# Performance work log

Hardware: AMD Instinct MI355X
Metric: run time of the kernel (lower is better)

The kernel has to match this reference:

```python
import jax, jax.numpy as jnp
import numpy as np

B, Cin, H, W = 8, 256, 32, 32
KS, NH, K = 32, 8, 5          # key_size == value_size, num_heads, kernel_size
STRIDE, PAD = 1, 2
Cout = KS * 3 * NH            # 768
EPS = 1e-5


def setup_inputs() -> dict:
    key = jax.random.key(0)
    k0, k1, k2 = jax.random.split(key, 3)
    return {
        "x": jax.random.normal(k0, (B, Cin, H, W), jnp.float32),
        "conv_w": jax.random.normal(k1, (Cout, Cin), jnp.float32) / np.sqrt(Cin).astype(np.float32),
        "conv_b": jax.random.normal(k2, (Cout,), jnp.float32) * 0.02,
        "gn_w": jnp.ones((Cout,), jnp.float32),
        "gn_b": jnp.zeros((Cout,), jnp.float32),
    }


def reference(x, conv_w, conv_b, gn_w, gn_b):
    Bb = x.shape[0]
    OH = (H + 2 * PAD - K) // STRIDE + 1
    OW = (W + 2 * PAD - K) // STRIDE + 1

    # 1x1 conv: (B, Cout, H, W)
    attn = jnp.einsum('bchw,oc->bohw', x, conv_w) + conv_b[None, :, None, None]

    # unfold / Tile2d -> (B, KH, KW, Cout, OH, OW)
    ap = jnp.pad(attn, ((0, 0), (0, 0), (PAD, PAD), (PAD, PAD)))
    rows = []
    for kh in range(K):
        cols = [ap[:, :, kh:kh + OH * STRIDE:STRIDE, kw:kw + OW * STRIDE:STRIDE]
                for kw in range(K)]
        rows.append(jnp.stack(cols, axis=1))          # (B, KW, C, OH, OW)
    tiles = jnp.stack(rows, axis=1)                   # (B, KH, KW, C, OH, OW)

    # GroupNorm over (group_channels, OH, OW) per (b, kh, kw) sample.
    # groups = 3*NH, group size = KS (each head's key/query/value chunk).
    G = 3 * NH
    t = tiles.reshape(Bb, K, K, G, KS, OH, OW)
    mean = t.mean(axis=(4, 5, 6), keepdims=True)
    var = t.var(axis=(4, 5, 6), keepdims=True)        # biased, like torch GroupNorm
    t = (t - mean) * jax.lax.rsqrt(var + EPS)
    t = t.reshape(Bb, K, K, Cout, OH, OW)
    t = t * gn_w[None, None, None, :, None, None] + gn_b[None, None, None, :, None, None]

    # (B, OH, OW, NH, 3*KS, KH*KW)
    t = t.transpose(0, 4, 5, 3, 1, 2).reshape(Bb, OH, OW, NH, 3 * KS, K * K)
    keyt = t[..., :KS, :]            # (B, OH, OW, NH, KS, KK)
    qt = t[..., KS:2 * KS, :]
    vt = t[..., 2 * KS:, :]          # (B, OH, OW, NH, VS, KK)

    q = qt.mean(axis=-1)             # mean query over the window: (B, OH, OW, NH, KS)
    sal = jnp.einsum('bijnk,bijnkp->bijnp', q, keyt) / np.float32(np.sqrt(KS))
    mask = jax.nn.softmax(sal, axis=-1)               # (B, OH, OW, NH, KK)
    out = jnp.einsum('bijnvp,bijnp->bijnv', vt, mask)  # (B, OH, OW, NH, VS)

    out = out.transpose(0, 3, 4, 1, 2).reshape(Bb, NH * KS, OH, OW)
    return out
```

## Files before the change

kernel.cpp:

```cpp
#include <hip/hip_runtime.h>
#include <hip/hip_bf16.h>

#define B_    8
#define CIN   256
#define COUT  768
#define G_    24
#define PW    40
#define PLANE 1440
#define EPS_  1e-5f

typedef float f32x4 __attribute__((ext_vector_type(4)));
typedef short s16x8 __attribute__((ext_vector_type(8)));
typedef unsigned short ushort_t;
typedef unsigned short u16x4 __attribute__((ext_vector_type(4)));
typedef unsigned long long ull_t;

#define LDS_FENCE() do { asm volatile("" ::: "memory"); \
                         __builtin_amdgcn_s_waitcnt(0xC07F); \
                         asm volatile("" ::: "memory"); } while (0)

static __device__ __forceinline__ ushort_t f2bf(float f) {
    union { float f; unsigned u; } a; a.f = f;
    const unsigned u = a.u;
    const unsigned r = u + 0x7FFFu + ((u >> 16) & 1u);
    return (ushort_t)(r >> 16);
}
static __device__ __forceinline__ float bf2f(ushort_t h) {
    union { unsigned u; float f; } a; a.u = ((unsigned)h) << 16; return a.f;
}
static __device__ __forceinline__ void st4(float* dst, u16x4 v) {
    *(f32x4*)dst = f32x4{ bf2f(v[0]), bf2f(v[1]), bf2f(v[2]), bf2f(v[3]) };
}
static __device__ __forceinline__ unsigned pk2(float lo, float hi) {
    return (unsigned)f2bf(lo) | ((unsigned)f2bf(hi) << 16);
}

__launch_bounds__(256)
__global__ void conv_gemm(const float* __restrict__ wsrc, const float* __restrict__ x,
                          const float* __restrict__ bias, ushort_t* __restrict__ attn,
                          float* __restrict__ rowAgg) {
    const int t = threadIdx.x;
    const int wv = t >> 6, lane = t & 63;
    const int q = lane >> 4, l15 = lane & 15;
    const int m0 = blockIdx.y * 64;
    const int mw = wv * 16;
    const int n_t = blockIdx.x * 64;
    const int b = n_t >> 10, nl0 = n_t & 1023;
    const int y0 = nl0 >> 5;

    __shared__ ushort_t Bs[64][264];
    ushort_t (*Ct)[2][44] = (ushort_t (*)[2][44])(&Bs[0][0]);
    float (*red)[11]      = (float (*)[11])((char*)(&Bs[0][0]) + 64 * 2 * 44 * 2);

    {
        const int half = t >> 7;
        const int kp = t & 127;
        const int k2 = kp * 2;
        const float* xr0 = x + (size_t)b * (CIN * 1024) + (size_t)k2 * 1024 + nl0 + half * 32;
        const float* xr1 = xr0 + 1024;
        #pragma unroll
        for (int c = 0; c < 8; ++c) {
            const float4 u0 = *(const float4*)(xr0 + c * 4);
            const float4 u1 = *(const float4*)(xr1 + c * 4);
            const int nn = half * 32 + c * 4;
            *(unsigned*)&Bs[nn + 0][k2] = pk2(u0.x, u1.x);
            *(unsigned*)&Bs[nn + 1][k2] = pk2(u0.y, u1.y);
            *(unsigned*)&Bs[nn + 2][k2] = pk2(u0.z, u1.z);
            *(unsigned*)&Bs[nn + 3][k2] = pk2(u0.w, u1.w);
        }
    }
    __syncthreads();

    const float* aPf = wsrc + (size_t)(m0 + mw + l15) * 256 + q * 8;

    f32x4 acc[4] = {{0,0,0,0},{0,0,0,0},{0,0,0,0},{0,0,0,0}};
    #pragma unroll
    for (int k0 = 0; k0 < 256; k0 += 32) {
        const float4 af0 = *(const float4*)(aPf + k0);
        const float4 af1 = *(const float4*)(aPf + k0 + 4);
        s16x8 a;
        a[0] = (short)f2bf(af0.x); a[1] = (short)f2bf(af0.y);
        a[2] = (short)f2bf(af0.z); a[3] = (short)f2bf(af0.w);
        a[4] = (short)f2bf(af1.x); a[5] = (short)f2bf(af1.y);
        a[6] = (short)f2bf(af1.z); a[7] = (short)f2bf(af1.w);
        const int kk = k0 + q * 8;
        const s16x8 b0 = *(const s16x8*)&Bs[l15 +  0][kk];
        const s16x8 b1 = *(const s16x8*)&Bs[l15 + 16][kk];
        const s16x8 b2 = *(const s16x8*)&Bs[l15 + 32][kk];
        const s16x8 b3 = *(const s16x8*)&Bs[l15 + 48][kk];
        acc[0] = __builtin_amdgcn_mfma_f32_16x16x32_bf16(a, b0, acc[0], 0, 0, 0);
        acc[1] = __builtin_amdgcn_mfma_f32_16x16x32_bf16(a, b1, acc[1], 0, 0, 0);
        acc[2] = __builtin_amdgcn_mfma_f32_16x16x32_bf16(a, b2, acc[2], 0, 0, 0);
        acc[3] = __builtin_amdgcn_mfma_f32_16x16x32_bf16(a, b3, acc[3], 0, 0, 0);
    }
    __syncthreads();

    float bb[4];
    #pragma unroll
    for (int r = 0; r < 4; ++r) bb[r] = bias[m0 + mw + q * 4 + r];
    #pragma unroll
    for (int j = 0; j < 4; ++j) {
        const int yy = j >> 1, xx = (j & 1) * 16 + l15;
        #pragma unroll
        for (int r = 0; r < 4; ++r)
            Ct[mw + q * 4 + r][yy][2 + xx] = f2bf(acc[j][r] + bb[r]);
    }
    #pragma unroll
    for (int it = 0; it < 2; ++it) {
        const int id = it * 256 + t;
        const int m = id >> 3, yy = (id >> 2) & 1, pos = id & 3;
        const int us = (pos == 0) ? 0 : (32 + 2 * pos);
        *(unsigned*)&Ct[m][yy][us] = 0u;
    }
    __syncthreads();

    ushort_t* pb = attn + ((size_t)(b * COUT + m0)) * PLANE;
    #pragma unroll
    for (int it = 0; it < 5; ++it) {
        const int id = it * 256 + t;
        const int m = id / 20, rem = id % 20, yy = rem / 10, s = rem % 10;
        const ull_t v = *(const ull_t*)&Ct[m][yy][s * 4];
        *(ull_t*)(pb + (size_t)m * PLANE + (y0 + yy + 2) * PW + s * 4) = v;
    }
    if (y0 == 0 || y0 == 30) {
        const int rowA = (y0 == 0) ? 0 : 34;
        #pragma unroll
        for (int it = 0; it < 5; ++it) {
            const int id = it * 256 + t;
            const int m = id / 20, rem = id % 20, yy = rem / 10, s = rem % 10;
            *(ull_t*)(pb + (size_t)m * PLANE + (rowA + yy) * PW + s * 4) = 0ull;
        }
    }

    if (t < 128) {
        const int gi = t >> 6, yy = (t >> 5) & 1, c = t & 31;
        const int m = gi * 32 + c;
        float lin = 0.f, sq = 0.f, e0 = 0.f, e1 = 0.f, e30 = 0.f, e31 = 0.f;
        #pragma unroll
        for (int u = 0; u < 9; ++u) {
            const ull_t vv = *(const ull_t*)&Ct[m][yy][u * 4];
            const unsigned lo = (unsigned)vv, hi = (unsigned)(vv >> 32);
            union { unsigned u; float f; } f0, f1, f2, f3;
            f0.u = lo << 16; f1.u = lo & 0xffff0000u;
            f2.u = hi << 16; f3.u = hi & 0xffff0000u;
            lin += (f0.f + f1.f) + (f2.f + f3.f);
            sq  += (f0.f * f0.f + f1.f * f1.f) + (f2.f * f2.f + f3.f * f3.f);
            if (u == 0) { e0 = f2.f; e1 = f3.f; }
            if (u == 8) { e30 = f0.f; e31 = f1.f; }
        }
        red[t][0] = lin; red[t][1] = sq;
        red[t][2] = e0;  red[t][3] = e0 * e0;
        red[t][4] = e1;  red[t][5] = e1 * e1;
        red[t][6] = e30; red[t][7] = e30 * e30;
        red[t][8] = e31; red[t][9] = e31 * e31;
    }
    __syncthreads();
    if (t < 40) {
        const int s = t % 10, gy = t / 10;
        const int gi = gy >> 1, yy = gy & 1;
        float sum = 0.f;
        #pragma unroll
        for (int c = 0; c < 32; ++c) sum += red[gi * 64 + yy * 32 + c][s];
        const int g = blockIdx.y * 2 + gi;
        rowAgg[(((size_t)b * G_ + g) * 32 + (y0 + yy)) * 10 + s] = sum;
    }
}

__launch_bounds__(128)
__global__ void local_attn(const ushort_t* __restrict__ attn,
                           const float* __restrict__ rowAgg,
                           const float* __restrict__ gn_w, const float* __restrict__ gn_b,
                           float* __restrict__ out) {
    const int wid = blockIdx.x;
    const int b = wid >> 7;
    const int n = (wid >> 4) & 7;
    const int i0 = (wid & 15) * 2;
    const int t = threadIdx.x;
    const int h = t >> 6;
    const int lane = t & 63;
    const int r = lane >> 5;
    const int j = lane & 31;

    __shared__ float KB[2][2][240];
    __shared__ float QB[2][2][240];
    __shared__ float ex[128][27];
    __shared__ float rpL[96][5], rp2L[96][5];
    __shared__ float s_m[75], s_r[75];
    __shared__ float s_rq[25], s_mq[25], s_rk[25], s_ck[25], s_rv[25], s_cv[25];
    __shared__ float s_gw[96], s_gb[96];

    if (t < 96) { s_gw[t] = gn_w[n * 96 + t]; s_gb[t] = gn_b[n * 96 + t]; }

    const float* rab = rowAgg + (size_t)((b * G_ + n * 3) * 32) * 10;
    if (t < 96) {
        const float* a = rab + (size_t)t * 10;
        const float S = a[0], Sq = a[1];
        const float e0 = a[2], q0 = a[3], e1 = a[4], q1 = a[5];
        const float e30 = a[6], q30 = a[7], e31 = a[8], q31 = a[9];
        rpL[t][0] = S - e30 - e31; rpL[t][1] = S - e31; rpL[t][2] = S;
        rpL[t][3] = S - e0;        rpL[t][4] = S - e0 - e1;
        rp2L[t][0] = Sq - q30 - q31; rp2L[t][1] = Sq - q31; rp2L[t][2] = Sq;
        rp2L[t][3] = Sq - q0;        rp2L[t][4] = Sq - q0 - q1;
    }
    __syncthreads();

    if (t < 75) {
        const int gi = t / 25, p = t % 25;
        const int kw = p % 5, kh = p / 5;
        const int rb = gi * 32;
        float cs = 0.f, cs2 = 0.f;
        #pragma unroll
        for (int yy = 0; yy < 32; ++yy) { cs += rpL[rb + yy][kw]; cs2 += rp2L[rb + yy][kw]; }
        if (kh == 0)      { cs -= rpL[rb + 30][kw] + rpL[rb + 31][kw]; cs2 -= rp2L[rb + 30][kw] + rp2L[rb + 31][kw]; }
        else if (kh == 1) { cs -= rpL[rb + 31][kw];                    cs2 -= rp2L[rb + 31][kw]; }
        else if (kh == 3) { cs -= rpL[rb + 0][kw];                     cs2 -= rp2L[rb + 0][kw]; }
        else if (kh == 4) { cs -= rpL[rb + 0][kw] + rpL[rb + 1][kw];   cs2 -= rp2L[rb + 0][kw] + rp2L[rb + 1][kw]; }
        const float inv_n = 1.f / 32768.f;
        const float mean = cs * inv_n;
        const float var  = cs2 * inv_n - mean * mean;
        s_m[t] = mean;
        s_r[t] = rsqrtf(var + EPS_);
    }
    __syncthreads();

    if (t < 25) {
        const float mK = s_m[t],      rK = s_r[t];
        const float mQ = s_m[25 + t], rQ = s_r[25 + t];
        const float mV = s_m[50 + t], rV = s_r[50 + t];
        s_rk[t] = rK; s_ck[t] = mK * rK;
        s_rq[t] = rQ; s_mq[t] = mQ * rQ;
        s_rv[t] = rV; s_cv[t] = mV * rV;
    }
    __syncthreads();

    float rq[25]; float cQ = 0.f;
    #pragma unroll
    for (int p = 0; p < 25; ++p) { rq[p] = s_rq[p]; cQ += s_mq[p]; }

    const ushort_t* regB = attn + (size_t)(b * COUT + n * 96) * PLANE + i0 * PW;
    const bool stg = (lane < 60);
    const int eo = lane * 4;
    const int base = r * PW + j;

    const ushort_t* baseK = regB + (size_t)(h * 16) * PLANE;
    const ushort_t* baseQ = regB + (size_t)(32 + h * 16) * PLANE;
    const ushort_t* baseV = regB + (size_t)(64 + h * 16) * PLANE;

    u16x4 nK{0,0,0,0}, nQ{0,0,0,0}, fK{0,0,0,0}, fQ{0,0,0,0};
    if (stg) {
        const u16x4 c0K = *(const u16x4*)(baseK + eo);
        const u16x4 c0Q = *(const u16x4*)(baseQ + eo);
        st4(&KB[h][0][eo], c0K);
        st4(&QB[h][0][eo], c0Q);
        nK = *(const u16x4*)(baseK + (size_t)PLANE + eo);
        nQ = *(const u16x4*)(baseQ + (size_t)PLANE + eo);
        fK = *(const u16x4*)(baseK + 2 * (size_t)PLANE + eo);
        fQ = *(const u16x4*)(baseQ + 2 * (size_t)PLANE + eo);
    }
    LDS_FENCE();

    float sal[25];
    #pragma unroll
    for (int p = 0; p < 25; ++p) sal[p] = 0.f;
    float sumQ2 = 0.f, sumQB = 0.f;

    for (int cc = 0; cc < 16; ++cc) {
        const int buf = cc & 1;
        if (stg && cc < 15) {
            st4(&KB[h][buf ^ 1][eo], nK);
            st4(&QB[h][buf ^ 1][eo], nQ);
            nK = fK; nQ = fQ;
            if (cc < 13) {
                fK = *(const u16x4*)(baseK + (size_t)(cc + 3) * PLANE + eo);
                fQ = *(const u16x4*)(baseQ + (size_t)(cc + 3) * PLANE + eo);
            } else if (cc == 13) {
                fK = *(const u16x4*)(baseV + eo);
                fQ = *(const u16x4*)(baseV + (size_t)PLANE + eo);
            }
        }
        const int ch = h * 16 + cc;
        const float* qb = &QB[h][buf][base];
        const float* kb = &KB[h][buf][base];
        float qa0 = 0.f, qa1 = 0.f, qa2 = 0.f, qa3 = 0.f, qa4 = 0.f;
        #pragma unroll
        for (int kw = 0; kw < 5; ++kw) {
            qa0 += rq[0 * 5 + kw] * qb[0 * PW + kw];
            qa1 += rq[1 * 5 + kw] * qb[1 * PW + kw];
            qa2 += rq[2 * 5 + kw] * qb[2 * PW + kw];
            qa3 += rq[3 * 5 + kw] * qb[3 * PW + kw];
            qa4 += rq[4 * 5 + kw] * qb[4 * PW + kw];
        }
        const float qa = (qa0 + qa1) + (qa2 + qa3) + qa4;
        const float qk  = s_gw[32 + ch] * ((qa - cQ) * 0.04f) + s_gb[32 + ch];
        const float qk2 = qk * s_gw[ch];
        sumQ2 += qk2; sumQB += qk * s_gb[ch];
        #pragma unroll
        for (int kh = 0; kh < 5; ++kh)
            #pragma unroll
            for (int kw = 0; kw < 5; ++kw)
                sal[kh * 5 + kw] += qk2 * kb[kh * PW + kw];
        LDS_FENCE();
    }

    #pragma unroll
    for (int p = 0; p < 25; ++p) ex[t][p] = sal[p];
    ex[t][25] = sumQ2; ex[t][26] = sumQB;
    if (stg) st4(&KB[h][0][eo], nK);
    __syncthreads();
    const int par = t ^ 64;
    #pragma unroll
    for (int p = 0; p < 25; ++p) sal[p] += ex[par][p];
    sumQ2 += ex[par][25]; sumQB += ex[par][26];

    u16x4 vA = nQ, vB{0,0,0,0};
    if (stg) vB = *(const u16x4*)(baseV + 2 * (size_t)PLANE + eo);

    #pragma unroll
    for (int p = 0; p < 25; ++p) sal[p] = s_rk[p] * sal[p] - s_ck[p] * sumQ2 + sumQB;

    const float scale = 0.17677669529663687f;
    float mmax = -3.4e38f;
    #pragma unroll
    for (int p = 0; p < 25; ++p) { sal[p] *= scale; mmax = fmaxf(mmax, sal[p]); }
    float ssum = 0.f;
    #pragma unroll
    for (int p = 0; p < 25; ++p) { sal[p] = __expf(sal[p] - mmax); ssum += sal[p]; }
    const float rs = 1.f / ssum;
    float cV2 = 0.f;
    #pragma unroll
    for (int p = 0; p < 25; ++p) {
        const float m = sal[p] * rs;
        sal[p] = m * s_rv[p];
        cV2 += m * s_cv[p];
    }
    LDS_FENCE();

    for (int cc = 0; cc < 16; ++cc) {
        const int buf = cc & 1;
        if (stg && cc < 15) {
            st4(&KB[h][buf ^ 1][eo], vA);
            vA = vB;
            if (cc < 13) vB = *(const u16x4*)(baseV + (size_t)(cc + 3) * PLANE + eo);
        }
        const int v = h * 16 + cc;
        const float* vb = &KB[h][buf][base];
        float a0 = 0.f, a1 = 0.f, a2 = 0.f, a3 = 0.f, a4 = 0.f;
        #pragma unroll
        for (int kw = 0; kw < 5; ++kw) {
            a0 += sal[0 * 5 + kw] * vb[0 * PW + kw];
            a1 += sal[1 * 5 + kw] * vb[1 * PW + kw];
            a2 += sal[2 * 5 + kw] * vb[2 * PW + kw];
            a3 += sal[3 * 5 + kw] * vb[3 * PW + kw];
            a4 += sal[4 * 5 + kw] * vb[4 * PW + kw];
        }
        const float acc = (a0 + a1) + (a2 + a3) + a4;
        out[((size_t)(b * 256 + n * 32 + v) * 32 + (i0 + r)) * 32 + j] =
            s_gw[64 + v] * acc + (s_gb[64 + v] - s_gw[64 + v] * cV2);
        LDS_FENCE();
    }
}

extern "C" void kernel_launch(void* const* d_in, const int* in_sizes, int n_in,
                              void* d_out, int out_size, void* d_ws, size_t ws_size,
                              hipStream_t stream) {
    const float* x      = (const float*)d_in[0];
    const float* conv_w = (const float*)d_in[1];
    const float* conv_b = (const float*)d_in[2];
    const float* gn_w   = (const float*)d_in[3];
    const float* gn_b   = (const float*)d_in[4];
    float* out = (float*)d_out;

    ushort_t* attn    = (ushort_t*)d_ws;
    float*    rowAgg  = (float*)(attn + 8847360);

    conv_gemm<<<dim3(128, 12), 256, 0, stream>>>(conv_w, x, conv_b, attn, rowAgg);
    local_attn<<<1024, 128, 0, stream>>>(attn, rowAgg, gn_w, gn_b, out);
}
```

Before: 118.1 us.

## Split local_attn channel loop across four waves instead of two

```diff
diff --git a/kernel.cpp b/kernel.cpp
--- a/kernel.cpp
+++ b/kernel.cpp
@@ -166,7 +166,7 @@
     }
 }
 
-__launch_bounds__(128)
+__launch_bounds__(256, 4)
 __global__ void local_attn(const ushort_t* __restrict__ attn,
                            const float* __restrict__ rowAgg,
                            const float* __restrict__ gn_w, const float* __restrict__ gn_b,
@@ -176,13 +176,13 @@
     const int n = (wid >> 4) & 7;
     const int i0 = (wid & 15) * 2;
     const int t = threadIdx.x;
-    const int h = t >> 6;
+    const int w = t >> 6;
     const int lane = t & 63;
     const int r = lane >> 5;
     const int j = lane & 31;
 
-    __shared__ float KB[2][2][240];
-    __shared__ float QB[2][2][240];
+    __shared__ float KB[4][2][240];
+    __shared__ float QB[4][2][240];
     __shared__ float ex[128][27];
     __shared__ float rpL[96][5], rp2L[96][5];
     __shared__ float s_m[75], s_r[75];
@@ -242,16 +242,16 @@
     const int eo = lane * 4;
     const int base = r * PW + j;
 
-    const ushort_t* baseK = regB + (size_t)(h * 16) * PLANE;
-    const ushort_t* baseQ = regB + (size_t)(32 + h * 16) * PLANE;
-    const ushort_t* baseV = regB + (size_t)(64 + h * 16) * PLANE;
+    const ushort_t* baseK = regB + (size_t)(w * 8) * PLANE;
+    const ushort_t* baseQ = regB + (size_t)(32 + w * 8) * PLANE;
+    const ushort_t* baseV = regB + (size_t)(64 + w * 8) * PLANE;
 
     u16x4 nK{0,0,0,0}, nQ{0,0,0,0}, fK{0,0,0,0}, fQ{0,0,0,0};
     if (stg) {
         const u16x4 c0K = *(const u16x4*)(baseK + eo);
         const u16x4 c0Q = *(const u16x4*)(baseQ + eo);
-        st4(&KB[h][0][eo], c0K);
-        st4(&QB[h][0][eo], c0Q);
+        st4(&KB[w][0][eo], c0K);
+        st4(&QB[w][0][eo], c0Q);
         nK = *(const u16x4*)(baseK + (size_t)PLANE + eo);
         nQ = *(const u16x4*)(baseQ + (size_t)PLANE + eo);
         fK = *(const u16x4*)(baseK + 2 * (size_t)PLANE + eo);
@@ -264,23 +264,23 @@
     for (int p = 0; p < 25; ++p) sal[p] = 0.f;
     float sumQ2 = 0.f, sumQB = 0.f;
 
-    for (int cc = 0; cc < 16; ++cc) {
+    for (int cc = 0; cc < 8; ++cc) {
         const int buf = cc & 1;
-        if (stg && cc < 15) {
-            st4(&KB[h][buf ^ 1][eo], nK);
-            st4(&QB[h][buf ^ 1][eo], nQ);
+        if (stg && cc < 7) {
+            st4(&KB[w][buf ^ 1][eo], nK);
+            st4(&QB[w][buf ^ 1][eo], nQ);
             nK = fK; nQ = fQ;
-            if (cc < 13) {
+            if (cc < 5) {
                 fK = *(const u16x4*)(baseK + (size_t)(cc + 3) * PLANE + eo);
                 fQ = *(const u16x4*)(baseQ + (size_t)(cc + 3) * PLANE + eo);
-            } else if (cc == 13) {
+            } else if (cc == 5) {
                 fK = *(const u16x4*)(baseV + eo);
                 fQ = *(const u16x4*)(baseV + (size_t)PLANE + eo);
             }
         }
-        const int ch = h * 16 + cc;
-        const float* qb = &QB[h][buf][base];
-        const float* kb = &KB[h][buf][base];
+        const int ch = w * 8 + cc;
+        const float* qb = &QB[w][buf][base];
+        const float* kb = &KB[w][buf][base];
         float qa0 = 0.f, qa1 = 0.f, qa2 = 0.f, qa3 = 0.f, qa4 = 0.f;
         #pragma unroll
         for (int kw = 0; kw < 5; ++kw) {
@@ -302,15 +302,35 @@
         LDS_FENCE();
     }
 
-    #pragma unroll
-    for (int p = 0; p < 25; ++p) ex[t][p] = sal[p];
-    ex[t][25] = sumQ2; ex[t][26] = sumQB;
-    if (stg) st4(&KB[h][0][eo], nK);
-    __syncthreads();
-    const int par = t ^ 64;
-    #pragma unroll
-    for (int p = 0; p < 25; ++p) sal[p] += ex[par][p];
-    sumQ2 += ex[par][25]; sumQB += ex[par][26];
+    if (stg) st4(&KB[w][0][eo], nK);
+    if (t >= 128) {
+        #pragma unroll
+        for (int p = 0; p < 25; ++p) ex[t - 128][p] = sal[p];
+        ex[t - 128][25] = sumQ2; ex[t - 128][26] = sumQB;
+    }
+    __syncthreads();
+    if (t < 128) {
+        #pragma unroll
+        for (int p = 0; p < 25; ++p) sal[p] += ex[t][p];
+        sumQ2 += ex[t][25]; sumQB += ex[t][26];
+        #pragma unroll
+        for (int p = 0; p < 25; ++p) ex[t][p] = sal[p];
+        ex[t][25] = sumQ2; ex[t][26] = sumQB;
+    }
+    __syncthreads();
+    {
+        const int l = t & 127;
+        if (t < 128) {
+            #pragma unroll
+            for (int p = 0; p < 25; ++p) sal[p] += ex[l ^ 64][p];
+            sumQ2 += ex[l ^ 64][25]; sumQB += ex[l ^ 64][26];
+        } else {
+            #pragma unroll
+            for (int p = 0; p < 25; ++p) sal[p] = ex[l][p] + ex[l ^ 64][p];
+            sumQ2 = ex[l][25] + ex[l ^ 64][25];
+            sumQB = ex[l][26] + ex[l ^ 64][26];
+        }
+    }
 
     u16x4 vA = nQ, vB{0,0,0,0};
     if (stg) vB = *(const u16x4*)(baseV + 2 * (size_t)PLANE + eo);
@@ -335,15 +355,15 @@
     }
     LDS_FENCE();
 
-    for (int cc = 0; cc < 16; ++cc) {
+    for (int cc = 0; cc < 8; ++cc) {
         const int buf = cc & 1;
-        if (stg && cc < 15) {
-            st4(&KB[h][buf ^ 1][eo], vA);
+        if (stg && cc < 7) {
+            st4(&KB[w][buf ^ 1][eo], vA);
             vA = vB;
-            if (cc < 13) vB = *(const u16x4*)(baseV + (size_t)(cc + 3) * PLANE + eo);
-        }
-        const int v = h * 16 + cc;
-        const float* vb = &KB[h][buf][base];
+            if (cc < 5) vB = *(const u16x4*)(baseV + (size_t)(cc + 3) * PLANE + eo);
+        }
+        const int v = w * 8 + cc;
+        const float* vb = &KB[w][buf][base];
         float a0 = 0.f, a1 = 0.f, a2 = 0.f, a3 = 0.f, a4 = 0.f;
         #pragma unroll
         for (int kw = 0; kw < 5; ++kw) {
@@ -374,5 +394,5 @@
     float*    rowAgg  = (float*)(attn + 8847360);
 
     conv_gemm<<<dim3(128, 12), 256, 0, stream>>>(conv_w, x, conv_b, attn, rowAgg);
-    local_attn<<<1024, 128, 0, stream>>>(attn, rowAgg, gn_w, gn_b, out);
-}
+    local_attn<<<1024, 256, 0, stream>>>(attn, rowAgg, gn_w, gn_b, out);
+}
```

Result: slower. 337.5 us (+185.9%).
